# Kernel optimization log

Measured on AMD Instinct MI355X. Metric: run time of the kernel, lower is better.

## Reference

```python
import jax, jax.numpy as jnp
import numpy as np

B, F, S, H = 1024, 64, 512, 128


def setup_inputs() -> dict:
    key = jax.random.key(0)
    ks = jax.random.split(key, 9)
    x = jax.random.normal(ks[0], (B, F, S), dtype=jnp.float32)
    available_len = jax.random.randint(ks[1], (B,), 1, S // 2).astype(jnp.int32)
    extra = jax.random.randint(ks[2], (B,), 0, S // 2)
    predict_len = jnp.minimum(available_len + extra, S).astype(jnp.int32)
    s = 1.0 / float(np.sqrt(H))  # PyTorch default uniform init scale
    u = lambda k, shape: jax.random.uniform(k, shape, jnp.float32, -s, s)
    W_ih = u(ks[3], (4 * H, F))
    W_hh = u(ks[4], (4 * H, H))
    b_ih = u(ks[5], (4 * H,))
    b_hh = u(ks[6], (4 * H,))
    W_den = u(ks[7], (F, H))
    b_den = u(ks[8], (F,))
    init_ch = jnp.zeros((1, 2 * H), dtype=jnp.float32)  # nn.Parameter(zeros(1, 2*n_hidden))
    return {"x": x, "available_len": available_len, "predict_len": predict_len,
            "W_ih": W_ih, "W_hh": W_hh, "b_ih": b_ih, "b_hh": b_hh,
            "W_den": W_den, "b_den": b_den, "init_ch": init_ch}


def reference(x, available_len, predict_len, W_ih, W_hh, b_ih, b_hh, W_den, b_den, init_ch):
    """Masked autoregressive LSTMCell recurrence.

    Row r is active at step t iff t < predict_len[r]; once inactive it never
    re-activates (the torch code's per-step gather of c_1/h_1 by predict_len is
    exactly this monotone-shrinking active set, expressed here as a masked
    full-batch state update). For t >= available_len[r] (and still active) the
    input is the model's own previous prediction (auto-regression feedback).
    Returns the permuted buffer (seq_len, batch, n_fea), matching the torch code.
    """
    Bb, Ff, Ss = x.shape
    Hh = W_hh.shape[1]
    xs = jnp.transpose(x, (2, 0, 1))  # (S, B, F)
    c0 = jnp.broadcast_to(init_ch[:, :Hh], (Bb, Hh))
    h0 = jnp.broadcast_to(init_ch[:, Hh:], (Bb, Hh))

    def step(carry, inp):
        h, c, prev_out = carry
        t, x_t = inp  # t: scalar step index, x_t: (B, F)
        sel = t < predict_len                       # active rows
        use_pred = (t >= available_len) & sel
        inp_t = jnp.where(use_pred[:, None], prev_out, x_t)
        gates = inp_t @ W_ih.T + b_ih + h @ W_hh.T + b_hh  # (B, 4H)
        i, f, g, o = jnp.split(gates, 4, axis=-1)
        c_new = jax.nn.sigmoid(f) * c + jax.nn.sigmoid(i) * jnp.tanh(g)
        h_new = jax.nn.sigmoid(o) * jnp.tanh(c_new)
        h = jnp.where(sel[:, None], h_new, h)
        c = jnp.where(sel[:, None], c_new, c)
        pred = h_new @ W_den.T + b_den              # (B, F)
        out_t = jnp.where(sel[:, None], pred, inp_t)  # x[t, sel] <- prediction
        return (h, c, out_t), out_t

    _, ys = jax.lax.scan(step, (h0, c0, jnp.zeros_like(xs[0])),
                         (jnp.arange(Ss), xs))
    return ys  # (S, B, F)
```

## Files before the change

### kernel.cpp

```cpp
#include <hip/hip_runtime.h>

#define BB 1024
#define FF 64
#define SS 512
#define HH 128
#define ZP 200
#define ZROWS 16

typedef __attribute__((ext_vector_type(8))) short bf16x8;
typedef __attribute__((ext_vector_type(4))) float f32x4;

__device__ __forceinline__ unsigned short f2bf(float f) {
    unsigned int u = __float_as_uint(f);
    u += 0x7fff + ((u >> 16) & 1);
    return (unsigned short)(u >> 16);
}

__device__ __forceinline__ bf16x8 pack8(const float* v) {
    bf16x8 r;
    #pragma unroll
    for (int i = 0; i < 8; i++) r[i] = (short)f2bf(v[i]);
    return r;
}

__global__ __launch_bounds__(512, 2)
void lstm_mfma_kernel(const float* __restrict__ x,
                      const int* __restrict__ available_len,
                      const int* __restrict__ predict_len,
                      const float* __restrict__ W_ih,
                      const float* __restrict__ W_hh,
                      const float* __restrict__ b_ih,
                      const float* __restrict__ b_hh,
                      const float* __restrict__ W_den,
                      const float* __restrict__ b_den,
                      const float* __restrict__ init_ch,
                      float* __restrict__ out)
{
    const int b0  = blockIdx.x * 4;
    const int tid = threadIdx.x;
    const int w   = tid >> 6;
    const int l   = tid & 63;
    const int l16 = l & 15;
    const int lq  = l >> 4;

    __shared__ __align__(16) unsigned short zbuf[2][ZROWS * ZP];

    for (int i = tid; i < 2 * ZROWS * ZP / 2; i += 512)
        ((unsigned int*)zbuf)[i] = 0u;

    const int p0 = predict_len[b0], p1 = predict_len[b0+1],
              p2 = predict_len[b0+2], p3 = predict_len[b0+3];
    const int maxP = max(max(p0, p1), max(p2, p3));
    const int P_my  = predict_len[b0 + lq];
    const int AV_my = available_len[b0 + lq];

    bf16x8 wg[4][6];
    float bias[4];
    #pragma unroll
    for (int g = 0; g < 4; ++g) {
        const int n = 128*g + 16*w + l16;
        const float* rih = W_ih + n * FF;
        const float* rhh = W_hh + n * HH;
        #pragma unroll
        for (int kt = 0; kt < 6; ++kt) {
            const int k = 32*kt + 8*lq;
            const float* src = (k < 64) ? (rih + k) : (rhh + (k - 64));
            float tmp[8];
            #pragma unroll
            for (int i = 0; i < 8; i++) tmp[i] = src[i];
            wg[g][kt] = pack8(tmp);
        }
        bias[g] = b_ih[n] + b_hh[n];
    }

    bf16x8 wd0, wd1, wd2, wd3;
    float bden = 0.f;
    size_t xbase = 0;
    int AV_x = 0;
    if (w < 4) {
        const int f = 16*w + l16;
        const float* rd = W_den + f * HH;
        float tmp[8];
        #pragma unroll
        for (int i = 0; i < 8; i++) tmp[i] = rd[0*32 + 8*lq + i];
        wd0 = pack8(tmp);
        #pragma unroll
        for (int i = 0; i < 8; i++) tmp[i] = rd[1*32 + 8*lq + i];
        wd1 = pack8(tmp);
        #pragma unroll
        for (int i = 0; i < 8; i++) tmp[i] = rd[2*32 + 8*lq + i];
        wd2 = pack8(tmp);
        #pragma unroll
        for (int i = 0; i < 8; i++) tmp[i] = rd[3*32 + 8*lq + i];
        wd3 = pack8(tmp);
        bden = b_den[f];
        xbase = ((size_t)(b0 + w) * FF + l) * SS;
        AV_x  = available_len[b0 + w];
    }

    const int unit = 16*w + l16;
    float c = init_ch[unit];
    const float h0 = init_ch[HH + unit];

    __syncthreads();

    zbuf[0][(4*lq)*ZP + 64 + unit] = f2bf(h0);
    if (w < 4) {
        float xv0 = x[xbase + 0];
        zbuf[0][(4*w)*ZP + l] = f2bf(xv0);
    }

    int cur = 0;
    for (int t = 0; t < maxP; ++t) {
        __syncthreads();

        const unsigned short* zc = zbuf[cur];
        bf16x8 a0 = *(const bf16x8*)(zc + l16*ZP +   0 + 8*lq);
        bf16x8 a1 = *(const bf16x8*)(zc + l16*ZP +  32 + 8*lq);
        bf16x8 a2 = *(const bf16x8*)(zc + l16*ZP +  64 + 8*lq);
        bf16x8 a3 = *(const bf16x8*)(zc + l16*ZP +  96 + 8*lq);
        bf16x8 a4 = *(const bf16x8*)(zc + l16*ZP + 128 + 8*lq);
        bf16x8 a5 = *(const bf16x8*)(zc + l16*ZP + 160 + 8*lq);

        float xv = 0.f;
        const bool xload = (w < 4) && (t + 1 < AV_x);
        if (xload) xv = x[xbase + t + 1];

        float gate0, gate1, gate2, gate3;
        {
            f32x4 acc = {0.f, 0.f, 0.f, 0.f};
            acc = __builtin_amdgcn_mfma_f32_16x16x32_bf16(a0, wg[0][0], acc, 0,0,0);
            acc = __builtin_amdgcn_mfma_f32_16x16x32_bf16(a1, wg[0][1], acc, 0,0,0);
            acc = __builtin_amdgcn_mfma_f32_16x16x32_bf16(a2, wg[0][2], acc, 0,0,0);
            acc = __builtin_amdgcn_mfma_f32_16x16x32_bf16(a3, wg[0][3], acc, 0,0,0);
            acc = __builtin_amdgcn_mfma_f32_16x16x32_bf16(a4, wg[0][4], acc, 0,0,0);
            acc = __builtin_amdgcn_mfma_f32_16x16x32_bf16(a5, wg[0][5], acc, 0,0,0);
            gate0 = acc[0] + bias[0];
        }
        {
            f32x4 acc = {0.f, 0.f, 0.f, 0.f};
            acc = __builtin_amdgcn_mfma_f32_16x16x32_bf16(a0, wg[1][0], acc, 0,0,0);
            acc = __builtin_amdgcn_mfma_f32_16x16x32_bf16(a1, wg[1][1], acc, 0,0,0);
            acc = __builtin_amdgcn_mfma_f32_16x16x32_bf16(a2, wg[1][2], acc, 0,0,0);
            acc = __builtin_amdgcn_mfma_f32_16x16x32_bf16(a3, wg[1][3], acc, 0,0,0);
            acc = __builtin_amdgcn_mfma_f32_16x16x32_bf16(a4, wg[1][4], acc, 0,0,0);
            acc = __builtin_amdgcn_mfma_f32_16x16x32_bf16(a5, wg[1][5], acc, 0,0,0);
            gate1 = acc[0] + bias[1];
        }
        {
            f32x4 acc = {0.f, 0.f, 0.f, 0.f};
            acc = __builtin_amdgcn_mfma_f32_16x16x32_bf16(a0, wg[2][0], acc, 0,0,0);
            acc = __builtin_amdgcn_mfma_f32_16x16x32_bf16(a1, wg[2][1], acc, 0,0,0);
            acc = __builtin_amdgcn_mfma_f32_16x16x32_bf16(a2, wg[2][2], acc, 0,0,0);
            acc = __builtin_amdgcn_mfma_f32_16x16x32_bf16(a3, wg[2][3], acc, 0,0,0);
            acc = __builtin_amdgcn_mfma_f32_16x16x32_bf16(a4, wg[2][4], acc, 0,0,0);
            acc = __builtin_amdgcn_mfma_f32_16x16x32_bf16(a5, wg[2][5], acc, 0,0,0);
            gate2 = acc[0] + bias[2];
        }
        {
            f32x4 acc = {0.f, 0.f, 0.f, 0.f};
            acc = __builtin_amdgcn_mfma_f32_16x16x32_bf16(a0, wg[3][0], acc, 0,0,0);
            acc = __builtin_amdgcn_mfma_f32_16x16x32_bf16(a1, wg[3][1], acc, 0,0,0);
            acc = __builtin_amdgcn_mfma_f32_16x16x32_bf16(a2, wg[3][2], acc, 0,0,0);
            acc = __builtin_amdgcn_mfma_f32_16x16x32_bf16(a3, wg[3][3], acc, 0,0,0);
            acc = __builtin_amdgcn_mfma_f32_16x16x32_bf16(a4, wg[3][4], acc, 0,0,0);
            acc = __builtin_amdgcn_mfma_f32_16x16x32_bf16(a5, wg[3][5], acc, 0,0,0);
            gate3 = acc[0] + bias[3];
        }

        const float si = 1.f / (1.f + __expf(-gate0));
        const float sf = 1.f / (1.f + __expf(-gate1));
        const float tg = 1.f - 2.f / (__expf(2.f * gate2) + 1.f);
        const float so = 1.f / (1.f + __expf(-gate3));
        const float cn = sf * c + si * tg;
        const float tc = 1.f - 2.f / (__expf(2.f * cn) + 1.f);
        const float hn = so * tc;

        const bool sel = (t < P_my);
        if (sel) c = cn;

        const int nxt = cur ^ 1;
        if (sel) zbuf[nxt][(4*lq)*ZP + 64 + unit] = f2bf(hn);
        if (xload) zbuf[nxt][(4*w)*ZP + l] = f2bf(xv);

        __syncthreads();

        if (w < 4) {
            const unsigned short* zn = zbuf[nxt];
            bf16x8 h0f = *(const bf16x8*)(zn + l16*ZP + 64 +  0 + 8*lq);
            bf16x8 h1f = *(const bf16x8*)(zn + l16*ZP + 64 + 32 + 8*lq);
            bf16x8 h2f = *(const bf16x8*)(zn + l16*ZP + 64 + 64 + 8*lq);
            bf16x8 h3f = *(const bf16x8*)(zn + l16*ZP + 64 + 96 + 8*lq);
            f32x4 pacc = {0.f, 0.f, 0.f, 0.f};
            pacc = __builtin_amdgcn_mfma_f32_16x16x32_bf16(h0f, wd0, pacc, 0,0,0);
            pacc = __builtin_amdgcn_mfma_f32_16x16x32_bf16(h1f, wd1, pacc, 0,0,0);
            pacc = __builtin_amdgcn_mfma_f32_16x16x32_bf16(h2f, wd2, pacc, 0,0,0);
            pacc = __builtin_amdgcn_mfma_f32_16x16x32_bf16(h3f, wd3, pacc, 0,0,0);
            const float pred = pacc[0] + bden;
            if (t < P_my) {
                out[(size_t)t * BB * FF + (size_t)(b0 + lq) * FF + 16*w + l16] = pred;
                if (t + 1 >= AV_my && t + 1 < P_my)
                    zbuf[nxt][(4*lq)*ZP + 16*w + l16] = f2bf(pred);
            }
        }
        cur = nxt;
    }
}

__global__ void tail_copy(const float* __restrict__ x,
                          const int* __restrict__ predict_len,
                          float* __restrict__ out)
{
    __shared__ float tile[64][65];
    const int b  = blockIdx.x;
    const int t0 = blockIdx.y * 64;
    const int P  = predict_len[b];
    if (t0 + 64 <= P) return;

    const int tid = threadIdx.x;
    const int tt  = tid & 63;
    const int fb  = tid >> 6;
    #pragma unroll
    for (int i = 0; i < 16; i++) {
        int f = fb * 16 + i;
        tile[f][tt] = x[(size_t)b * FF * SS + (size_t)f * SS + t0 + tt];
    }
    __syncthreads();
    const int f2 = tid & 63;
    const int tb = tid >> 6;
    #pragma unroll
    for (int i = 0; i < 16; i++) {
        int tloc = tb * 16 + i;
        int t    = t0 + tloc;
        if (t >= P) out[(size_t)t * BB * FF + (size_t)b * FF + f2] = tile[f2][tloc];
    }
}

extern "C" void kernel_launch(void* const* d_in, const int* in_sizes, int n_in,
                              void* d_out, int out_size, void* d_ws, size_t ws_size,
                              hipStream_t stream) {
    const float* x       = (const float*)d_in[0];
    const int*   avail   = (const int*)  d_in[1];
    const int*   plen    = (const int*)  d_in[2];
    const float* W_ih    = (const float*)d_in[3];
    const float* W_hh    = (const float*)d_in[4];
    const float* b_ih    = (const float*)d_in[5];
    const float* b_hh    = (const float*)d_in[6];
    const float* W_den   = (const float*)d_in[7];
    const float* b_den   = (const float*)d_in[8];
    const float* init_ch = (const float*)d_in[9];
    float*       out     = (float*)d_out;

    tail_copy<<<dim3(BB, SS/64), dim3(256), 0, stream>>>(x, plen, out);
    lstm_mfma_kernel<<<dim3(BB/4), dim3(512), 0, stream>>>(
        x, avail, plen, W_ih, W_hh, b_ih, b_hh, W_den, b_den, init_ch, out);
}
```

Before: 484.7 us.

## Fold dense head into LSTM input weights to remove per-step barrier

A small pre-kernel computes W_ih·W_den and W_ih·b_den, and each row's autoregressive recurrence uses W_hh + W_ih·W_den applied to h, with h stored in a separate LDS column region. The output projection for step t-1 is computed from the same h operands in step t, so the second __syncthreads and the separate prediction phase per step are removed. Teacher and autoregressive MFMA groups are skipped when no row in the block needs them. The cost is more weight registers (10 k-tiles per gate), a wider LDS row, one extra loop iteration, and slightly different rounding because the folded weights are quantized to bf16.

```diff
diff --git a/kernel.cpp b/kernel.cpp
--- a/kernel.cpp
+++ b/kernel.cpp
@@ -4,7 +4,7 @@
 #define FF 64
 #define SS 512
 #define HH 128
-#define ZP 200
+#define ZP 328
 #define ZROWS 16
 
 typedef __attribute__((ext_vector_type(8))) short bf16x8;
@@ -16,11 +16,23 @@
     return (unsigned short)(u >> 16);
 }
 
-__device__ __forceinline__ bf16x8 pack8(const float* v) {
-    bf16x8 r;
-    #pragma unroll
-    for (int i = 0; i < 8; i++) r[i] = (short)f2bf(v[i]);
-    return r;
+__global__ void fold_kernel(const float* __restrict__ W_ih,
+                            const float* __restrict__ W_den,
+                            const float* __restrict__ b_den,
+                            float* __restrict__ ws)
+{
+    const int n = blockIdx.x;
+    const int k = threadIdx.x;
+    float s = 0.f;
+    #pragma unroll 8
+    for (int f = 0; f < FF; ++f) s = fmaf(W_ih[n*FF + f], W_den[f*HH + k], s);
+    ws[n*HH + k] = s;
+    if (k == 0) {
+        float bsum = 0.f;
+        #pragma unroll 8
+        for (int f = 0; f < FF; ++f) bsum = fmaf(W_ih[n*FF + f], b_den[f], bsum);
+        ws[4*HH*HH + n] = bsum;
+    }
 }
 
 __global__ __launch_bounds__(512, 2)
@@ -34,6 +46,7 @@
                       const float* __restrict__ W_den,
                       const float* __restrict__ b_den,
                       const float* __restrict__ init_ch,
+                      const float* __restrict__ ws,
                       float* __restrict__ out)
 {
     const int b0  = blockIdx.x * 4;
@@ -42,57 +55,76 @@
     const int l   = tid & 63;
     const int l16 = l & 15;
     const int lq  = l >> 4;
+    const bool w4 = (w < 4);
 
     __shared__ __align__(16) unsigned short zbuf[2][ZROWS * ZP];
 
     for (int i = tid; i < 2 * ZROWS * ZP / 2; i += 512)
         ((unsigned int*)zbuf)[i] = 0u;
 
+    const int a0v = available_len[b0], a1v = available_len[b0+1],
+              a2v = available_len[b0+2], a3v = available_len[b0+3];
     const int p0 = predict_len[b0], p1 = predict_len[b0+1],
               p2 = predict_len[b0+2], p3 = predict_len[b0+3];
-    const int maxP = max(max(p0, p1), max(p2, p3));
+    const int maxP  = max(max(p0, p1), max(p2, p3));
+    const int minAV = min(min(a0v, a1v), min(a2v, a3v));
+    const int maxAV = max(max(a0v, a1v), max(a2v, a3v));
     const int P_my  = predict_len[b0 + lq];
     const int AV_my = available_len[b0 + lq];
 
-    bf16x8 wg[4][6];
-    float bias[4];
+    bf16x8 wg[4][10];
+    float bias_t[4], bias_a[4];
+    const float* wfold = ws;
+    const float* bfold = ws + 4*HH*HH;
     #pragma unroll
     for (int g = 0; g < 4; ++g) {
         const int n = 128*g + 16*w + l16;
-        const float* rih = W_ih + n * FF;
-        const float* rhh = W_hh + n * HH;
-        #pragma unroll
-        for (int kt = 0; kt < 6; ++kt) {
-            const int k = 32*kt + 8*lq;
-            const float* src = (k < 64) ? (rih + k) : (rhh + (k - 64));
-            float tmp[8];
-            #pragma unroll
-            for (int i = 0; i < 8; i++) tmp[i] = src[i];
-            wg[g][kt] = pack8(tmp);
-        }
-        bias[g] = b_ih[n] + b_hh[n];
-    }
-
-    bf16x8 wd0, wd1, wd2, wd3;
+        const float* rih = W_ih  + n * FF;
+        const float* rhh = W_hh  + n * HH;
+        const float* rfo = wfold + n * HH;
+        #pragma unroll
+        for (int kt = 0; kt < 2; ++kt) {
+            const int k = 32*kt + 8*lq;
+            bf16x8 r;
+            #pragma unroll
+            for (int i = 0; i < 8; i++) r[i] = (short)f2bf(rih[k + i]);
+            wg[g][kt] = r;
+        }
+        #pragma unroll
+        for (int kt = 0; kt < 4; ++kt) {
+            const int k = 32*kt + 8*lq;
+            bf16x8 r;
+            #pragma unroll
+            for (int i = 0; i < 8; i++) r[i] = (short)f2bf(rhh[k + i]);
+            wg[g][2 + kt] = r;
+        }
+        #pragma unroll
+        for (int kt = 0; kt < 4; ++kt) {
+            const int k = 32*kt + 8*lq;
+            bf16x8 r;
+            #pragma unroll
+            for (int i = 0; i < 8; i++) r[i] = (short)f2bf(rhh[k + i] + rfo[k + i]);
+            wg[g][6 + kt] = r;
+        }
+        bias_t[g] = b_ih[n] + b_hh[n];
+        bias_a[g] = bias_t[g] + bfold[n];
+    }
+
+    bf16x8 wd[4];
     float bden = 0.f;
     size_t xbase = 0;
     int AV_x = 0;
-    if (w < 4) {
+    if (w4) {
         const int f = 16*w + l16;
         const float* rd = W_den + f * HH;
-        float tmp[8];
-        #pragma unroll
-        for (int i = 0; i < 8; i++) tmp[i] = rd[0*32 + 8*lq + i];
-        wd0 = pack8(tmp);
-        #pragma unroll
-        for (int i = 0; i < 8; i++) tmp[i] = rd[1*32 + 8*lq + i];
-        wd1 = pack8(tmp);
-        #pragma unroll
-        for (int i = 0; i < 8; i++) tmp[i] = rd[2*32 + 8*lq + i];
-        wd2 = pack8(tmp);
-        #pragma unroll
-        for (int i = 0; i < 8; i++) tmp[i] = rd[3*32 + 8*lq + i];
-        wd3 = pack8(tmp);
+        #pragma unroll
+        for (int kt = 0; kt < 4; ++kt) {
+            const int k = 32*kt + 8*lq;
+            bf16x8 r;
+            #pragma unroll
+            for (int i = 0; i < 8; i++) r[i] = (short)f2bf(rd[k + i]);
+            wd[kt] = r;
+        }
         bden = b_den[f];
         xbase = ((size_t)(b0 + w) * FF + l) * SS;
         AV_x  = available_len[b0 + w];
@@ -100,110 +132,102 @@
 
     const int unit = 16*w + l16;
     float c = init_ch[unit];
-    const float h0 = init_ch[HH + unit];
+    const float h0v = init_ch[HH + unit];
 
     __syncthreads();
 
-    zbuf[0][(4*lq)*ZP + 64 + unit] = f2bf(h0);
-    if (w < 4) {
-        float xv0 = x[xbase + 0];
-        zbuf[0][(4*w)*ZP + l] = f2bf(xv0);
-    }
+    zbuf[0][(4*lq)*ZP + 64 + unit] = f2bf(h0v);
+    if (w4) zbuf[0][(4*w)*ZP + l] = f2bf(x[xbase]);
 
     int cur = 0;
-    for (int t = 0; t < maxP; ++t) {
+    for (int t = 0; t <= maxP; ++t) {
         __syncthreads();
-
         const unsigned short* zc = zbuf[cur];
-        bf16x8 a0 = *(const bf16x8*)(zc + l16*ZP +   0 + 8*lq);
-        bf16x8 a1 = *(const bf16x8*)(zc + l16*ZP +  32 + 8*lq);
-        bf16x8 a2 = *(const bf16x8*)(zc + l16*ZP +  64 + 8*lq);
-        bf16x8 a3 = *(const bf16x8*)(zc + l16*ZP +  96 + 8*lq);
-        bf16x8 a4 = *(const bf16x8*)(zc + l16*ZP + 128 + 8*lq);
-        bf16x8 a5 = *(const bf16x8*)(zc + l16*ZP + 160 + 8*lq);
+        const bool anyT = (t < maxAV);
+        const bool anyA = (t >= minAV);
+        const bool last = (t == maxP);
+        const bool dop  = w4 && (t > 0);
+        const int abase = l16*ZP + 8*lq;
 
         float xv = 0.f;
-        const bool xload = (w < 4) && (t + 1 < AV_x);
-        if (xload) xv = x[xbase + t + 1];
-
-        float gate0, gate1, gate2, gate3;
-        {
-            f32x4 acc = {0.f, 0.f, 0.f, 0.f};
-            acc = __builtin_amdgcn_mfma_f32_16x16x32_bf16(a0, wg[0][0], acc, 0,0,0);
-            acc = __builtin_amdgcn_mfma_f32_16x16x32_bf16(a1, wg[0][1], acc, 0,0,0);
-            acc = __builtin_amdgcn_mfma_f32_16x16x32_bf16(a2, wg[0][2], acc, 0,0,0);
-            acc = __builtin_amdgcn_mfma_f32_16x16x32_bf16(a3, wg[0][3], acc, 0,0,0);
-            acc = __builtin_amdgcn_mfma_f32_16x16x32_bf16(a4, wg[0][4], acc, 0,0,0);
-            acc = __builtin_amdgcn_mfma_f32_16x16x32_bf16(a5, wg[0][5], acc, 0,0,0);
-            gate0 = acc[0] + bias[0];
-        }
-        {
-            f32x4 acc = {0.f, 0.f, 0.f, 0.f};
-            acc = __builtin_amdgcn_mfma_f32_16x16x32_bf16(a0, wg[1][0], acc, 0,0,0);
-            acc = __builtin_amdgcn_mfma_f32_16x16x32_bf16(a1, wg[1][1], acc, 0,0,0);
-            acc = __builtin_amdgcn_mfma_f32_16x16x32_bf16(a2, wg[1][2], acc, 0,0,0);
-            acc = __builtin_amdgcn_mfma_f32_16x16x32_bf16(a3, wg[1][3], acc, 0,0,0);
-            acc = __builtin_amdgcn_mfma_f32_16x16x32_bf16(a4, wg[1][4], acc, 0,0,0);
-            acc = __builtin_amdgcn_mfma_f32_16x16x32_bf16(a5, wg[1][5], acc, 0,0,0);
-            gate1 = acc[0] + bias[1];
-        }
-        {
-            f32x4 acc = {0.f, 0.f, 0.f, 0.f};
-            acc = __builtin_amdgcn_mfma_f32_16x16x32_bf16(a0, wg[2][0], acc, 0,0,0);
-            acc = __builtin_amdgcn_mfma_f32_16x16x32_bf16(a1, wg[2][1], acc, 0,0,0);
-            acc = __builtin_amdgcn_mfma_f32_16x16x32_bf16(a2, wg[2][2], acc, 0,0,0);
-            acc = __builtin_amdgcn_mfma_f32_16x16x32_bf16(a3, wg[2][3], acc, 0,0,0);
-            acc = __builtin_amdgcn_mfma_f32_16x16x32_bf16(a4, wg[2][4], acc, 0,0,0);
-            acc = __builtin_amdgcn_mfma_f32_16x16x32_bf16(a5, wg[2][5], acc, 0,0,0);
-            gate2 = acc[0] + bias[2];
-        }
-        {
-            f32x4 acc = {0.f, 0.f, 0.f, 0.f};
-            acc = __builtin_amdgcn_mfma_f32_16x16x32_bf16(a0, wg[3][0], acc, 0,0,0);
-            acc = __builtin_amdgcn_mfma_f32_16x16x32_bf16(a1, wg[3][1], acc, 0,0,0);
-            acc = __builtin_amdgcn_mfma_f32_16x16x32_bf16(a2, wg[3][2], acc, 0,0,0);
-            acc = __builtin_amdgcn_mfma_f32_16x16x32_bf16(a3, wg[3][3], acc, 0,0,0);
-            acc = __builtin_amdgcn_mfma_f32_16x16x32_bf16(a4, wg[3][4], acc, 0,0,0);
-            acc = __builtin_amdgcn_mfma_f32_16x16x32_bf16(a5, wg[3][5], acc, 0,0,0);
-            gate3 = acc[0] + bias[3];
-        }
-
-        const float si = 1.f / (1.f + __expf(-gate0));
-        const float sf = 1.f / (1.f + __expf(-gate1));
-        const float tg = 1.f - 2.f / (__expf(2.f * gate2) + 1.f);
-        const float so = 1.f / (1.f + __expf(-gate3));
-        const float cn = sf * c + si * tg;
-        const float tc = 1.f - 2.f / (__expf(2.f * cn) + 1.f);
-        const float hn = so * tc;
-
-        const bool sel = (t < P_my);
-        if (sel) c = cn;
-
-        const int nxt = cur ^ 1;
-        if (sel) zbuf[nxt][(4*lq)*ZP + 64 + unit] = f2bf(hn);
-        if (xload) zbuf[nxt][(4*w)*ZP + l] = f2bf(xv);
-
-        __syncthreads();
-
-        if (w < 4) {
-            const unsigned short* zn = zbuf[nxt];
-            bf16x8 h0f = *(const bf16x8*)(zn + l16*ZP + 64 +  0 + 8*lq);
-            bf16x8 h1f = *(const bf16x8*)(zn + l16*ZP + 64 + 32 + 8*lq);
-            bf16x8 h2f = *(const bf16x8*)(zn + l16*ZP + 64 + 64 + 8*lq);
-            bf16x8 h3f = *(const bf16x8*)(zn + l16*ZP + 64 + 96 + 8*lq);
-            f32x4 pacc = {0.f, 0.f, 0.f, 0.f};
-            pacc = __builtin_amdgcn_mfma_f32_16x16x32_bf16(h0f, wd0, pacc, 0,0,0);
-            pacc = __builtin_amdgcn_mfma_f32_16x16x32_bf16(h1f, wd1, pacc, 0,0,0);
-            pacc = __builtin_amdgcn_mfma_f32_16x16x32_bf16(h2f, wd2, pacc, 0,0,0);
-            pacc = __builtin_amdgcn_mfma_f32_16x16x32_bf16(h3f, wd3, pacc, 0,0,0);
-            const float pred = pacc[0] + bden;
-            if (t < P_my) {
-                out[(size_t)t * BB * FF + (size_t)(b0 + lq) * FF + 16*w + l16] = pred;
-                if (t + 1 >= AV_my && t + 1 < P_my)
-                    zbuf[nxt][(4*lq)*ZP + 16*w + l16] = f2bf(pred);
-            }
-        }
-        cur = nxt;
+        const bool xl = w4 && !last && (t + 1 < AV_x);
+        if (xl) xv = x[xbase + t + 1];
+
+        f32x4 pa  = {0.f,0.f,0.f,0.f};
+        f32x4 ac0 = {0.f,0.f,0.f,0.f}, ac1 = {0.f,0.f,0.f,0.f},
+              ac2 = {0.f,0.f,0.f,0.f}, ac3 = {0.f,0.f,0.f,0.f};
+
+        if (anyT) {
+            if (!last) {
+                bf16x8 a0 = *(const bf16x8*)(zc + abase + 0);
+                bf16x8 a1 = *(const bf16x8*)(zc + abase + 32);
+                ac0 = __builtin_amdgcn_mfma_f32_16x16x32_bf16(a0, wg[0][0], ac0, 0,0,0);
+                ac1 = __builtin_amdgcn_mfma_f32_16x16x32_bf16(a0, wg[1][0], ac1, 0,0,0);
+                ac2 = __builtin_amdgcn_mfma_f32_16x16x32_bf16(a0, wg[2][0], ac2, 0,0,0);
+                ac3 = __builtin_amdgcn_mfma_f32_16x16x32_bf16(a0, wg[3][0], ac3, 0,0,0);
+                ac0 = __builtin_amdgcn_mfma_f32_16x16x32_bf16(a1, wg[0][1], ac0, 0,0,0);
+                ac1 = __builtin_amdgcn_mfma_f32_16x16x32_bf16(a1, wg[1][1], ac1, 0,0,0);
+                ac2 = __builtin_amdgcn_mfma_f32_16x16x32_bf16(a1, wg[2][1], ac2, 0,0,0);
+                ac3 = __builtin_amdgcn_mfma_f32_16x16x32_bf16(a1, wg[3][1], ac3, 0,0,0);
+            }
+            #pragma unroll
+            for (int kt = 0; kt < 4; ++kt) {
+                bf16x8 v = *(const bf16x8*)(zc + abase + 64 + 32*kt);
+                if (dop) pa = __builtin_amdgcn_mfma_f32_16x16x32_bf16(v, wd[kt], pa, 0,0,0);
+                if (!last) {
+                    ac0 = __builtin_amdgcn_mfma_f32_16x16x32_bf16(v, wg[0][2+kt], ac0, 0,0,0);
+                    ac1 = __builtin_amdgcn_mfma_f32_16x16x32_bf16(v, wg[1][2+kt], ac1, 0,0,0);
+                    ac2 = __builtin_amdgcn_mfma_f32_16x16x32_bf16(v, wg[2][2+kt], ac2, 0,0,0);
+                    ac3 = __builtin_amdgcn_mfma_f32_16x16x32_bf16(v, wg[3][2+kt], ac3, 0,0,0);
+                }
+            }
+        }
+        if (anyA) {
+            #pragma unroll
+            for (int kt = 0; kt < 4; ++kt) {
+                bf16x8 v = *(const bf16x8*)(zc + abase + 192 + 32*kt);
+                if (dop) pa = __builtin_amdgcn_mfma_f32_16x16x32_bf16(v, wd[kt], pa, 0,0,0);
+                if (!last) {
+                    ac0 = __builtin_amdgcn_mfma_f32_16x16x32_bf16(v, wg[0][6+kt], ac0, 0,0,0);
+                    ac1 = __builtin_amdgcn_mfma_f32_16x16x32_bf16(v, wg[1][6+kt], ac1, 0,0,0);
+                    ac2 = __builtin_amdgcn_mfma_f32_16x16x32_bf16(v, wg[2][6+kt], ac2, 0,0,0);
+                    ac3 = __builtin_amdgcn_mfma_f32_16x16x32_bf16(v, wg[3][6+kt], ac3, 0,0,0);
+                }
+            }
+        }
+
+        if (dop && (t - 1 < P_my)) {
+            out[(size_t)(t-1) * BB * FF + (size_t)(b0 + lq) * FF + 16*w + l16] = pa[0] + bden;
+        }
+
+        if (!last) {
+            const bool auto_my = (t >= AV_my);
+            const float g0 = ac0[0] + (auto_my ? bias_a[0] : bias_t[0]);
+            const float g1 = ac1[0] + (auto_my ? bias_a[1] : bias_t[1]);
+            const float g2 = ac2[0] + (auto_my ? bias_a[2] : bias_t[2]);
+            const float g3 = ac3[0] + (auto_my ? bias_a[3] : bias_t[3]);
+
+            const float si = 1.f / (1.f + __expf(-g0));
+            const float sf = 1.f / (1.f + __expf(-g1));
+            const float tg = 1.f - 2.f / (__expf(2.f * g2) + 1.f);
+            const float so = 1.f / (1.f + __expf(-g3));
+            const float cn = sf * c + si * tg;
+            const float tc = 1.f - 2.f / (__expf(2.f * cn) + 1.f);
+            const float hn = so * tc;
+
+            const bool sel = (t < P_my);
+            if (sel) c = cn;
+
+            const int nxt = cur ^ 1;
+            const unsigned short hbf = f2bf(hn);
+            const bool teach_next = (t + 1 < AV_my);
+            if (sel) {
+                zbuf[nxt][(4*lq)*ZP +  64 + unit] = teach_next ? hbf : (unsigned short)0;
+                zbuf[nxt][(4*lq)*ZP + 192 + unit] = teach_next ? (unsigned short)0 : hbf;
+            }
+            if (w4) zbuf[nxt][(4*w)*ZP + l] = xl ? f2bf(xv) : (unsigned short)0;
+            cur = nxt;
+        }
     }
 }
 
@@ -250,8 +274,10 @@
     const float* b_den   = (const float*)d_in[8];
     const float* init_ch = (const float*)d_in[9];
     float*       out     = (float*)d_out;
-
+    float*       ws      = (float*)d_ws;
+
+    fold_kernel<<<dim3(4*HH), dim3(HH), 0, stream>>>(W_ih, W_den, b_den, ws);
     tail_copy<<<dim3(BB, SS/64), dim3(256), 0, stream>>>(x, plen, out);
     lstm_mfma_kernel<<<dim3(BB/4), dim3(512), 0, stream>>>(
-        x, avail, plen, W_ih, W_hh, b_ih, b_hh, W_den, b_den, init_ch, out);
-}
+        x, avail, plen, W_ih, W_hh, b_ih, b_hh, W_den, b_den, init_ch, ws, out);
+}
```

New measurement: 602.8 us. 1.24x slower.

## Interleave gate MFMA chains, defer prediction stores, relax occupancy hint

Applied to the files above, without the earlier changes.

The four dependent 6-deep MFMA chains become interleaved across four independent accumulators, so the matrix unit pipeline stays busy instead of stalling on each chain. The global store of each step's prediction moves to the start of the next step, taking it off the critical path before the barrier, and the final step's store is written after the loop. The launch bound changes from two blocks per CU to a waves-per-EU hint of 1, which gives the compiler more registers. The feedback write condition is also loosened to t < P_my, which may write one extra autoregressive value into shared memory.

```diff
diff --git a/kernel.cpp b/kernel.cpp
--- a/kernel.cpp
+++ b/kernel.cpp
@@ -16,14 +16,7 @@
     return (unsigned short)(u >> 16);
 }
 
-__device__ __forceinline__ bf16x8 pack8(const float* v) {
-    bf16x8 r;
-    #pragma unroll
-    for (int i = 0; i < 8; i++) r[i] = (short)f2bf(v[i]);
-    return r;
-}
-
-__global__ __launch_bounds__(512, 2)
+__global__ __launch_bounds__(512) __attribute__((amdgpu_waves_per_eu(1)))
 void lstm_mfma_kernel(const float* __restrict__ x,
                       const int* __restrict__ available_len,
                       const int* __restrict__ predict_len,
@@ -42,6 +35,7 @@
     const int l   = tid & 63;
     const int l16 = l & 15;
     const int lq  = l >> 4;
+    const bool w4 = (w < 4);
 
     __shared__ __align__(16) unsigned short zbuf[2][ZROWS * ZP];
 
@@ -50,7 +44,7 @@
 
     const int p0 = predict_len[b0], p1 = predict_len[b0+1],
               p2 = predict_len[b0+2], p3 = predict_len[b0+3];
-    const int maxP = max(max(p0, p1), max(p2, p3));
+    const int maxP  = max(max(p0, p1), max(p2, p3));
     const int P_my  = predict_len[b0 + lq];
     const int AV_my = available_len[b0 + lq];
 
@@ -65,10 +59,10 @@
         for (int kt = 0; kt < 6; ++kt) {
             const int k = 32*kt + 8*lq;
             const float* src = (k < 64) ? (rih + k) : (rhh + (k - 64));
-            float tmp[8];
+            bf16x8 r;
             #pragma unroll
-            for (int i = 0; i < 8; i++) tmp[i] = src[i];
-            wg[g][kt] = pack8(tmp);
+            for (int i = 0; i < 8; i++) r[i] = (short)f2bf(src[i]);
+            wg[g][kt] = r;
         }
         bias[g] = b_ih[n] + b_hh[n];
     }
@@ -77,22 +71,22 @@
     float bden = 0.f;
     size_t xbase = 0;
     int AV_x = 0;
-    if (w < 4) {
+    if (w4) {
         const int f = 16*w + l16;
         const float* rd = W_den + f * HH;
-        float tmp[8];
-        #pragma unroll
-        for (int i = 0; i < 8; i++) tmp[i] = rd[0*32 + 8*lq + i];
-        wd0 = pack8(tmp);
-        #pragma unroll
-        for (int i = 0; i < 8; i++) tmp[i] = rd[1*32 + 8*lq + i];
-        wd1 = pack8(tmp);
-        #pragma unroll
-        for (int i = 0; i < 8; i++) tmp[i] = rd[2*32 + 8*lq + i];
-        wd2 = pack8(tmp);
-        #pragma unroll
-        for (int i = 0; i < 8; i++) tmp[i] = rd[3*32 + 8*lq + i];
-        wd3 = pack8(tmp);
+        bf16x8 r;
+        #pragma unroll
+        for (int i = 0; i < 8; i++) r[i] = (short)f2bf(rd[0*32 + 8*lq + i]);
+        wd0 = r;
+        #pragma unroll
+        for (int i = 0; i < 8; i++) r[i] = (short)f2bf(rd[1*32 + 8*lq + i]);
+        wd1 = r;
+        #pragma unroll
+        for (int i = 0; i < 8; i++) r[i] = (short)f2bf(rd[2*32 + 8*lq + i]);
+        wd2 = r;
+        #pragma unroll
+        for (int i = 0; i < 8; i++) r[i] = (short)f2bf(rd[3*32 + 8*lq + i]);
+        wd3 = r;
         bden = b_den[f];
         xbase = ((size_t)(b0 + w) * FF + l) * SS;
         AV_x  = available_len[b0 + w];
@@ -100,78 +94,69 @@
 
     const int unit = 16*w + l16;
     float c = init_ch[unit];
-    const float h0 = init_ch[HH + unit];
+    const float h0v = init_ch[HH + unit];
 
     __syncthreads();
 
-    zbuf[0][(4*lq)*ZP + 64 + unit] = f2bf(h0);
-    if (w < 4) {
-        float xv0 = x[xbase + 0];
-        zbuf[0][(4*w)*ZP + l] = f2bf(xv0);
-    }
-
+    zbuf[0][(4*lq)*ZP + 64 + unit] = f2bf(h0v);
+    if (w4) zbuf[0][(4*w)*ZP + l] = f2bf(x[xbase]);
+
+    float predreg = 0.f;
     int cur = 0;
     for (int t = 0; t < maxP; ++t) {
         __syncthreads();
 
+        if (w4 && t > 0 && (t - 1) < P_my)
+            out[(size_t)(t-1) * BB * FF + (size_t)(b0 + lq) * FF + 16*w + l16] = predreg;
+
+        float xv = 0.f;
+        const bool xl = w4 && (t + 1 < AV_x);
+        if (xl) xv = x[xbase + t + 1];
+
         const unsigned short* zc = zbuf[cur];
-        bf16x8 a0 = *(const bf16x8*)(zc + l16*ZP +   0 + 8*lq);
-        bf16x8 a1 = *(const bf16x8*)(zc + l16*ZP +  32 + 8*lq);
-        bf16x8 a2 = *(const bf16x8*)(zc + l16*ZP +  64 + 8*lq);
-        bf16x8 a3 = *(const bf16x8*)(zc + l16*ZP +  96 + 8*lq);
-        bf16x8 a4 = *(const bf16x8*)(zc + l16*ZP + 128 + 8*lq);
-        bf16x8 a5 = *(const bf16x8*)(zc + l16*ZP + 160 + 8*lq);
-
-        float xv = 0.f;
-        const bool xload = (w < 4) && (t + 1 < AV_x);
-        if (xload) xv = x[xbase + t + 1];
-
-        float gate0, gate1, gate2, gate3;
-        {
-            f32x4 acc = {0.f, 0.f, 0.f, 0.f};
-            acc = __builtin_amdgcn_mfma_f32_16x16x32_bf16(a0, wg[0][0], acc, 0,0,0);
-            acc = __builtin_amdgcn_mfma_f32_16x16x32_bf16(a1, wg[0][1], acc, 0,0,0);
-            acc = __builtin_amdgcn_mfma_f32_16x16x32_bf16(a2, wg[0][2], acc, 0,0,0);
-            acc = __builtin_amdgcn_mfma_f32_16x16x32_bf16(a3, wg[0][3], acc, 0,0,0);
-            acc = __builtin_amdgcn_mfma_f32_16x16x32_bf16(a4, wg[0][4], acc, 0,0,0);
-            acc = __builtin_amdgcn_mfma_f32_16x16x32_bf16(a5, wg[0][5], acc, 0,0,0);
-            gate0 = acc[0] + bias[0];
-        }
-        {
-            f32x4 acc = {0.f, 0.f, 0.f, 0.f};
-            acc = __builtin_amdgcn_mfma_f32_16x16x32_bf16(a0, wg[1][0], acc, 0,0,0);
-            acc = __builtin_amdgcn_mfma_f32_16x16x32_bf16(a1, wg[1][1], acc, 0,0,0);
-            acc = __builtin_amdgcn_mfma_f32_16x16x32_bf16(a2, wg[1][2], acc, 0,0,0);
-            acc = __builtin_amdgcn_mfma_f32_16x16x32_bf16(a3, wg[1][3], acc, 0,0,0);
-            acc = __builtin_amdgcn_mfma_f32_16x16x32_bf16(a4, wg[1][4], acc, 0,0,0);
-            acc = __builtin_amdgcn_mfma_f32_16x16x32_bf16(a5, wg[1][5], acc, 0,0,0);
-            gate1 = acc[0] + bias[1];
-        }
-        {
-            f32x4 acc = {0.f, 0.f, 0.f, 0.f};
-            acc = __builtin_amdgcn_mfma_f32_16x16x32_bf16(a0, wg[2][0], acc, 0,0,0);
-            acc = __builtin_amdgcn_mfma_f32_16x16x32_bf16(a1, wg[2][1], acc, 0,0,0);
-            acc = __builtin_amdgcn_mfma_f32_16x16x32_bf16(a2, wg[2][2], acc, 0,0,0);
-            acc = __builtin_amdgcn_mfma_f32_16x16x32_bf16(a3, wg[2][3], acc, 0,0,0);
-            acc = __builtin_amdgcn_mfma_f32_16x16x32_bf16(a4, wg[2][4], acc, 0,0,0);
-            acc = __builtin_amdgcn_mfma_f32_16x16x32_bf16(a5, wg[2][5], acc, 0,0,0);
-            gate2 = acc[0] + bias[2];
-        }
-        {
-            f32x4 acc = {0.f, 0.f, 0.f, 0.f};
-            acc = __builtin_amdgcn_mfma_f32_16x16x32_bf16(a0, wg[3][0], acc, 0,0,0);
-            acc = __builtin_amdgcn_mfma_f32_16x16x32_bf16(a1, wg[3][1], acc, 0,0,0);
-            acc = __builtin_amdgcn_mfma_f32_16x16x32_bf16(a2, wg[3][2], acc, 0,0,0);
-            acc = __builtin_amdgcn_mfma_f32_16x16x32_bf16(a3, wg[3][3], acc, 0,0,0);
-            acc = __builtin_amdgcn_mfma_f32_16x16x32_bf16(a4, wg[3][4], acc, 0,0,0);
-            acc = __builtin_amdgcn_mfma_f32_16x16x32_bf16(a5, wg[3][5], acc, 0,0,0);
-            gate3 = acc[0] + bias[3];
-        }
-
-        const float si = 1.f / (1.f + __expf(-gate0));
-        const float sf = 1.f / (1.f + __expf(-gate1));
-        const float tg = 1.f - 2.f / (__expf(2.f * gate2) + 1.f);
-        const float so = 1.f / (1.f + __expf(-gate3));
+        const int abase = l16*ZP + 8*lq;
+        bf16x8 a0 = *(const bf16x8*)(zc + abase +   0);
+        bf16x8 a1 = *(const bf16x8*)(zc + abase +  32);
+        bf16x8 a2 = *(const bf16x8*)(zc + abase +  64);
+        bf16x8 a3 = *(const bf16x8*)(zc + abase +  96);
+        bf16x8 a4 = *(const bf16x8*)(zc + abase + 128);
+        bf16x8 a5 = *(const bf16x8*)(zc + abase + 160);
+
+        f32x4 ac0 = {0.f,0.f,0.f,0.f}, ac1 = {0.f,0.f,0.f,0.f},
+              ac2 = {0.f,0.f,0.f,0.f}, ac3 = {0.f,0.f,0.f,0.f};
+        ac0 = __builtin_amdgcn_mfma_f32_16x16x32_bf16(a0, wg[0][0], ac0, 0,0,0);
+        ac1 = __builtin_amdgcn_mfma_f32_16x16x32_bf16(a0, wg[1][0], ac1, 0,0,0);
+        ac2 = __builtin_amdgcn_mfma_f32_16x16x32_bf16(a0, wg[2][0], ac2, 0,0,0);
+        ac3 = __builtin_amdgcn_mfma_f32_16x16x32_bf16(a0, wg[3][0], ac3, 0,0,0);
+        ac0 = __builtin_amdgcn_mfma_f32_16x16x32_bf16(a1, wg[0][1], ac0, 0,0,0);
+        ac1 = __builtin_amdgcn_mfma_f32_16x16x32_bf16(a1, wg[1][1], ac1, 0,0,0);
+        ac2 = __builtin_amdgcn_mfma_f32_16x16x32_bf16(a1, wg[2][1], ac2, 0,0,0);
+        ac3 = __builtin_amdgcn_mfma_f32_16x16x32_bf16(a1, wg[3][1], ac3, 0,0,0);
+        ac0 = __builtin_amdgcn_mfma_f32_16x16x32_bf16(a2, wg[0][2], ac0, 0,0,0);
+        ac1 = __builtin_amdgcn_mfma_f32_16x16x32_bf16(a2, wg[1][2], ac1, 0,0,0);
+        ac2 = __builtin_amdgcn_mfma_f32_16x16x32_bf16(a2, wg[2][2], ac2, 0,0,0);
+        ac3 = __builtin_amdgcn_mfma_f32_16x16x32_bf16(a2, wg[3][2], ac3, 0,0,0);
+        ac0 = __builtin_amdgcn_mfma_f32_16x16x32_bf16(a3, wg[0][3], ac0, 0,0,0);
+        ac1 = __builtin_amdgcn_mfma_f32_16x16x32_bf16(a3, wg[1][3], ac1, 0,0,0);
+        ac2 = __builtin_amdgcn_mfma_f32_16x16x32_bf16(a3, wg[2][3], ac2, 0,0,0);
+        ac3 = __builtin_amdgcn_mfma_f32_16x16x32_bf16(a3, wg[3][3], ac3, 0,0,0);
+        ac0 = __builtin_amdgcn_mfma_f32_16x16x32_bf16(a4, wg[0][4], ac0, 0,0,0);
+        ac1 = __builtin_amdgcn_mfma_f32_16x16x32_bf16(a4, wg[1][4], ac1, 0,0,0);
+        ac2 = __builtin_amdgcn_mfma_f32_16x16x32_bf16(a4, wg[2][4], ac2, 0,0,0);
+        ac3 = __builtin_amdgcn_mfma_f32_16x16x32_bf16(a4, wg[3][4], ac3, 0,0,0);
+        ac0 = __builtin_amdgcn_mfma_f32_16x16x32_bf16(a5, wg[0][5], ac0, 0,0,0);
+        ac1 = __builtin_amdgcn_mfma_f32_16x16x32_bf16(a5, wg[1][5], ac1, 0,0,0);
+        ac2 = __builtin_amdgcn_mfma_f32_16x16x32_bf16(a5, wg[2][5], ac2, 0,0,0);
+        ac3 = __builtin_amdgcn_mfma_f32_16x16x32_bf16(a5, wg[3][5], ac3, 0,0,0);
+
+        const float g0 = ac0[0] + bias[0];
+        const float g1 = ac1[0] + bias[1];
+        const float g2 = ac2[0] + bias[2];
+        const float g3 = ac3[0] + bias[3];
+        const float si = 1.f / (1.f + __expf(-g0));
+        const float sf = 1.f / (1.f + __expf(-g1));
+        const float tg = 1.f - 2.f / (__expf(2.f * g2) + 1.f);
+        const float so = 1.f / (1.f + __expf(-g3));
         const float cn = sf * c + si * tg;
         const float tc = 1.f - 2.f / (__expf(2.f * cn) + 1.f);
         const float hn = so * tc;
@@ -181,30 +166,29 @@
 
         const int nxt = cur ^ 1;
         if (sel) zbuf[nxt][(4*lq)*ZP + 64 + unit] = f2bf(hn);
-        if (xload) zbuf[nxt][(4*w)*ZP + l] = f2bf(xv);
+        if (xl)  zbuf[nxt][(4*w)*ZP + l] = f2bf(xv);
 
         __syncthreads();
 
-        if (w < 4) {
+        if (w4) {
             const unsigned short* zn = zbuf[nxt];
-            bf16x8 h0f = *(const bf16x8*)(zn + l16*ZP + 64 +  0 + 8*lq);
-            bf16x8 h1f = *(const bf16x8*)(zn + l16*ZP + 64 + 32 + 8*lq);
-            bf16x8 h2f = *(const bf16x8*)(zn + l16*ZP + 64 + 64 + 8*lq);
-            bf16x8 h3f = *(const bf16x8*)(zn + l16*ZP + 64 + 96 + 8*lq);
-            f32x4 pacc = {0.f, 0.f, 0.f, 0.f};
-            pacc = __builtin_amdgcn_mfma_f32_16x16x32_bf16(h0f, wd0, pacc, 0,0,0);
-            pacc = __builtin_amdgcn_mfma_f32_16x16x32_bf16(h1f, wd1, pacc, 0,0,0);
-            pacc = __builtin_amdgcn_mfma_f32_16x16x32_bf16(h2f, wd2, pacc, 0,0,0);
-            pacc = __builtin_amdgcn_mfma_f32_16x16x32_bf16(h3f, wd3, pacc, 0,0,0);
-            const float pred = pacc[0] + bden;
-            if (t < P_my) {
-                out[(size_t)t * BB * FF + (size_t)(b0 + lq) * FF + 16*w + l16] = pred;
-                if (t + 1 >= AV_my && t + 1 < P_my)
-                    zbuf[nxt][(4*lq)*ZP + 16*w + l16] = f2bf(pred);
-            }
+            bf16x8 h0f = *(const bf16x8*)(zn + abase + 64 +  0);
+            bf16x8 h1f = *(const bf16x8*)(zn + abase + 64 + 32);
+            bf16x8 h2f = *(const bf16x8*)(zn + abase + 64 + 64);
+            bf16x8 h3f = *(const bf16x8*)(zn + abase + 64 + 96);
+            f32x4 pa = {0.f,0.f,0.f,0.f};
+            pa = __builtin_amdgcn_mfma_f32_16x16x32_bf16(h0f, wd0, pa, 0,0,0);
+            pa = __builtin_amdgcn_mfma_f32_16x16x32_bf16(h1f, wd1, pa, 0,0,0);
+            pa = __builtin_amdgcn_mfma_f32_16x16x32_bf16(h2f, wd2, pa, 0,0,0);
+            pa = __builtin_amdgcn_mfma_f32_16x16x32_bf16(h3f, wd3, pa, 0,0,0);
+            predreg = pa[0] + bden;
+            if (t + 1 >= AV_my && t < P_my)
+                zbuf[nxt][(4*lq)*ZP + 16*w + l16] = f2bf(predreg);
         }
         cur = nxt;
     }
+    if (w4 && (maxP - 1) < P_my)
+        out[(size_t)(maxP-1) * BB * FF + (size_t)(b0 + lq) * FF + 16*w + l16] = predreg;
 }
 
 __global__ void tail_copy(const float* __restrict__ x,
```

New measurement: 551.7 us. 13.8% more time.
